# Optimization experiments

Hardware: AMD Instinct MI355X
Metric: run time of the kernel (lower is better)

The kernel has to match this reference:

```python
import jax, jax.numpy as jnp
import numpy as np

N = 8192
D_IN, D_H, D_OUT = 512, 256, 128
BETA = 0.8
EPS = 1e-08


def _xavier(key, fan_in, fan_out):
    limit = float(np.sqrt(6.0 / (fan_in + fan_out)))
    return jax.random.uniform(key, (fan_in, fan_out), jnp.float32, -limit, limit)


def setup_inputs() -> dict:
    key = jax.random.key(0)
    kA, kS, kx, kw1, kw2 = jax.random.split(key, 5)
    A = jax.random.uniform(kA, (N, N), jnp.float32)
    S = jax.random.uniform(kS, (N, N), jnp.float32)
    x = jax.random.normal(kx, (N, D_IN), jnp.float32)
    W1 = _xavier(kw1, D_IN, D_H)
    b1 = jnp.zeros((D_H,), jnp.float32)
    W2 = _xavier(kw2, D_H, D_OUT)
    b2 = jnp.zeros((D_OUT,), jnp.float32)
    return {"A": A, "S": S, "x": x, "W1": W1, "b1": b1, "W2": W2, "b2": b2}


def _normalize_adj(adj):
    # adj + eps * I  (add only on the diagonal; no dense eye materialized)
    idx = jnp.arange(adj.shape[0])
    adj = adj.at[idx, idx].add(EPS)
    d = adj.sum(axis=1)                       # [N]
    d_inv_sqrt = d ** -0.5
    d_inv_sqrt = jnp.where(jnp.isinf(d_inv_sqrt), 0.0, d_inv_sqrt)
    # D^{-1/2} A D^{-1/2} as broadcast row/col scaling (same math as diag matmuls)
    return d_inv_sqrt[:, None] * adj * d_inv_sqrt[None, :]


def reference(A, S, x, W1, b1, W2, b2):
    A_tilde = A + BETA * S                    # [N, N]
    A_norm = _normalize_adj(A_tilde)          # [N, N]
    # GCN layer 1: relu(A_norm @ (x @ W1) + b1)   (dropout is identity at eval)
    h = jax.nn.relu(A_norm @ (x @ W1) + b1)   # [N, D_H]
    # GCN layer 2 (output layer, no activation)
    out = A_norm @ (h @ W2) + b2              # [N, D_OUT]
    return out
```

## Files before the change

### kernel.cpp

```cpp
#include <hip/hip_runtime.h>

#define EPS 1e-8f
#define BETA 0.8f

typedef __attribute__((ext_vector_type(8))) short bf16x8;
typedef __attribute__((ext_vector_type(4))) float f32x4;
typedef __attribute__((ext_vector_type(4))) float float4v;
typedef __attribute__((ext_vector_type(4))) unsigned short ushort4v;

__device__ __forceinline__ unsigned short f2b(float f) {
  unsigned int u = __builtin_bit_cast(unsigned int, f);
  u += 0x7fffu + ((u >> 16) & 1u);
  return (unsigned short)(u >> 16);
}
__device__ __forceinline__ float b2f(unsigned short u) {
  unsigned int x = (unsigned int)u << 16;
  return __builtin_bit_cast(float, x);
}

__global__ __launch_bounds__(256) void k_degree_conv(
    const float* __restrict__ A, const float* __restrict__ S,
    unsigned short* __restrict__ At, float* __restrict__ dis,
    const float* __restrict__ x, unsigned short* __restrict__ xb,
    const float* __restrict__ W1, unsigned short* __restrict__ W1T,
    const float* __restrict__ W2, unsigned short* __restrict__ W2T) {
  __shared__ float wsum[4];
  const int tid = threadIdx.x;
  if (blockIdx.x < 8192) {
    const int row = blockIdx.x;
    const size_t base = (size_t)row * 8192;
    float4v a[8], s[8];
#pragma unroll
    for (int i = 0; i < 8; ++i) {
      const int c = i * 1024 + tid * 4;
      a[i] = __builtin_nontemporal_load(
          reinterpret_cast<const float4v*>(A + base + c));
      s[i] = __builtin_nontemporal_load(
          reinterpret_cast<const float4v*>(S + base + c));
    }
    float sum = 0.f;
#pragma unroll
    for (int i = 0; i < 8; ++i) {
      const int c = i * 1024 + tid * 4;
      float v0 = a[i].x + BETA * s[i].x;
      float v1 = a[i].y + BETA * s[i].y;
      float v2 = a[i].z + BETA * s[i].z;
      float v3 = a[i].w + BETA * s[i].w;
      sum += (v0 + v1) + (v2 + v3);
      ushort4v o = {f2b(v0), f2b(v1), f2b(v2), f2b(v3)};
      *reinterpret_cast<ushort4v*>(At + base + c) = o;
    }
#pragma unroll
    for (int off = 32; off > 0; off >>= 1) sum += __shfl_xor(sum, off, 64);
    if ((tid & 63) == 0) wsum[tid >> 6] = sum;
    __syncthreads();
    if (tid == 0) {
      float d = ((wsum[0] + wsum[1]) + (wsum[2] + wsum[3])) + EPS;
      dis[row] = (d > 0.f) ? 1.0f / sqrtf(d) : 0.f;
    }
  } else {
    const int b = blockIdx.x - 8192;
    if (b < 4096) {
      const int idx = b * 256 + tid;
      float4v v = reinterpret_cast<const float4v*>(x)[idx];
      ushort4v o = {f2b(v.x), f2b(v.y), f2b(v.z), f2b(v.w)};
      reinterpret_cast<ushort4v*>(xb)[idx] = o;
    } else if (b < 4608) {
      const int idx = (b - 4096) * 256 + tid;
      const int r = idx >> 8, c = idx & 255;
      W1T[c * 512 + r] = f2b(W1[idx]);
    } else {
      const int idx = (b - 4608) * 256 + tid;
      const int r = idx >> 7, c = idx & 127;
      W2T[c * 256 + r] = f2b(W2[idx]);
    }
  }
}

__global__ __launch_bounds__(256) void k_conv_all(
    const float* __restrict__ x, unsigned short* __restrict__ xb,
    const float* __restrict__ W1, unsigned short* __restrict__ W1T,
    const float* __restrict__ W2, unsigned short* __restrict__ W2T) {
  const int b = blockIdx.x;
  if (b < 4096) {
    const int idx = b * 256 + threadIdx.x;
    float4v v = reinterpret_cast<const float4v*>(x)[idx];
    ushort4v o = {f2b(v.x), f2b(v.y), f2b(v.z), f2b(v.w)};
    reinterpret_cast<ushort4v*>(xb)[idx] = o;
  } else if (b < 4608) {
    const int idx = (b - 4096) * 256 + threadIdx.x;
    const int r = idx >> 8, c = idx & 255;
    W1T[c * 512 + r] = f2b(W1[idx]);
  } else {
    const int idx = (b - 4608) * 256 + threadIdx.x;
    const int r = idx >> 7, c = idx & 127;
    W2T[c * 256 + r] = f2b(W2[idx]);
  }
}

__global__ __launch_bounds__(256) void k_degree_convert(
    const float* __restrict__ A, const float* __restrict__ S,
    unsigned short* __restrict__ At, float* __restrict__ dis) {
  const int row = blockIdx.x;
  const int tid = threadIdx.x;
  const size_t base = (size_t)row * 8192;
  float4v a[8], s[8];
#pragma unroll
  for (int i = 0; i < 8; ++i) {
    const int c = i * 1024 + tid * 4;
    a[i] = __builtin_nontemporal_load(
        reinterpret_cast<const float4v*>(A + base + c));
    s[i] = __builtin_nontemporal_load(
        reinterpret_cast<const float4v*>(S + base + c));
  }
  float sum = 0.f;
#pragma unroll
  for (int i = 0; i < 8; ++i) {
    const int c = i * 1024 + tid * 4;
    float v0 = a[i].x + BETA * s[i].x;
    float v1 = a[i].y + BETA * s[i].y;
    float v2 = a[i].z + BETA * s[i].z;
    float v3 = a[i].w + BETA * s[i].w;
    sum += (v0 + v1) + (v2 + v3);
    ushort4v o = {f2b(v0), f2b(v1), f2b(v2), f2b(v3)};
    *reinterpret_cast<ushort4v*>(At + base + c) = o;
  }
#pragma unroll
  for (int off = 32; off > 0; off >>= 1) sum += __shfl_xor(sum, off, 64);
  __shared__ float wsum[4];
  if ((tid & 63) == 0) wsum[tid >> 6] = sum;
  __syncthreads();
  if (tid == 0) {
    float d = ((wsum[0] + wsum[1]) + (wsum[2] + wsum[3])) + EPS;
    dis[row] = (d > 0.f) ? 1.0f / sqrtf(d) : 0.f;
  }
}

template <int BM, int BN, int EPI>
__global__ __launch_bounds__(256) void k_gemm_bt(
    const unsigned short* __restrict__ Ag, const unsigned short* __restrict__ BTg,
    int M, int N, int Kstride, int Kchunk,
    const float* __restrict__ dis, const float* __restrict__ bias,
    float* __restrict__ outf, unsigned short* __restrict__ outb) {
  constexpr int WM = BM / 2, WN = BN / 2;
  constexpr int MF = WM / 16, NF = WN / 16;
  constexpr int NLOADS = BM / 32 + BN / 32;
  __shared__ unsigned short Als[2][BM][64];
  __shared__ unsigned short Bls[2][BN][64];
  const int tid = threadIdx.x;
  const int lane = tid & 63;
  const int wm = (tid >> 6) >> 1, wn = (tid >> 6) & 1;
  const int brow = blockIdx.x * BM, bcol = blockIdx.y * BN;
  const int ar = tid >> 3;
  const int ac = (tid & 7) * 8;
  const int l15 = lane & 15, lk = (lane >> 4) * 8;

  f32x4 acc[MF][NF];
#pragma unroll
  for (int i = 0; i < MF; ++i)
#pragma unroll
    for (int j = 0; j < NF; ++j) acc[i][j] = (f32x4){0.f, 0.f, 0.f, 0.f};

  auto stage = [&](int buf, int k0) {
#pragma unroll
    for (int i = 0; i < BM / 32; ++i) {
      const unsigned short* g =
          Ag + (size_t)(brow + i * 32 + ar) * Kstride + k0 + ac;
      __builtin_amdgcn_global_load_lds(
          (const __attribute__((address_space(1))) void*)g,
          (__attribute__((address_space(3))) void*)&Als[buf][i * 32 + ar][ac],
          16, 0, 0);
    }
#pragma unroll
    for (int i = 0; i < BN / 32; ++i) {
      const unsigned short* g =
          BTg + (size_t)(bcol + i * 32 + ar) * Kstride + k0 + ac;
      __builtin_amdgcn_global_load_lds(
          (const __attribute__((address_space(1))) void*)g,
          (__attribute__((address_space(3))) void*)&Bls[buf][i * 32 + ar][ac],
          16, 0, 0);
    }
  };

  const int nsteps = Kchunk / 64;
  stage(0, 0);
  for (int t = 0; t < nsteps; ++t) {
    const int cur = t & 1;
    if (t + 1 < nsteps) {
      stage(cur ^ 1, (t + 1) * 64);
      asm volatile("s_waitcnt vmcnt(%0)" ::"n"(NLOADS));
    } else {
      asm volatile("s_waitcnt vmcnt(0)");
    }
    __builtin_amdgcn_s_barrier();
    asm volatile("" ::: "memory");
#pragma unroll
    for (int kk = 0; kk < 2; ++kk) {
      bf16x8 afr[MF], bfr[NF];
#pragma unroll
      for (int mi = 0; mi < MF; ++mi)
        afr[mi] = *reinterpret_cast<const bf16x8*>(
            &Als[cur][wm * WM + mi * 16 + l15][kk * 32 + lk]);
#pragma unroll
      for (int ni = 0; ni < NF; ++ni)
        bfr[ni] = *reinterpret_cast<const bf16x8*>(
            &Bls[cur][wn * WN + ni * 16 + l15][kk * 32 + lk]);
#pragma unroll
      for (int mi = 0; mi < MF; ++mi)
#pragma unroll
        for (int ni = 0; ni < NF; ++ni)
          acc[mi][ni] = __builtin_amdgcn_mfma_f32_16x16x32_bf16(
              afr[mi], bfr[ni], acc[mi][ni], 0, 0, 0);
    }
    asm volatile("" ::: "memory");
    __builtin_amdgcn_s_barrier();
  }

  const int crow0 = brow + wm * WM, ccol0 = bcol + wn * WN;
#pragma unroll
  for (int mi = 0; mi < MF; ++mi) {
    const int row0 = crow0 + mi * 16 + (lane >> 4) * 4;
    const float d0 = dis[row0], d1 = dis[row0 + 1], d2 = dis[row0 + 2],
                d3 = dis[row0 + 3];
#pragma unroll
    for (int ni = 0; ni < NF; ++ni) {
      const int col = ccol0 + ni * 16 + l15;
      f32x4 a = acc[mi][ni];
      if constexpr (EPI == 0) {
        ushort4v o = {f2b(d0 * a.x), f2b(d1 * a.y), f2b(d2 * a.z),
                      f2b(d3 * a.w)};
        *reinterpret_cast<ushort4v*>(outb + (size_t)col * M + row0) = o;
      } else if constexpr (EPI == 1) {
        const float bb = bias[col];
        float v0 = d0 * a.x + bb; v0 = v0 > 0.f ? v0 : 0.f;
        float v1 = d1 * a.y + bb; v1 = v1 > 0.f ? v1 : 0.f;
        float v2 = d2 * a.z + bb; v2 = v2 > 0.f ? v2 : 0.f;
        float v3 = d3 * a.w + bb; v3 = v3 > 0.f ? v3 : 0.f;
        outb[(size_t)(row0 + 0) * N + col] = f2b(v0);
        outb[(size_t)(row0 + 1) * N + col] = f2b(v1);
        outb[(size_t)(row0 + 2) * N + col] = f2b(v2);
        outb[(size_t)(row0 + 3) * N + col] = f2b(v3);
      } else {
        const float bb = bias[col];
        outf[(size_t)(row0 + 0) * N + col] = d0 * a.x + bb;
        outf[(size_t)(row0 + 1) * N + col] = d1 * a.y + bb;
        outf[(size_t)(row0 + 2) * N + col] = d2 * a.z + bb;
        outf[(size_t)(row0 + 3) * N + col] = d3 * a.w + bb;
      }
    }
  }
}

__global__ __launch_bounds__(512, 4) void k_gemm_big(
    const unsigned short* __restrict__ Ag,
    const unsigned short* __restrict__ BTg,
    int N, int Kchunk, int gx, int ncol,
    unsigned short* __restrict__ P) {
  constexpr int M = 8192, Kstride = 8192;
  constexpr int NLOADS = 4;
  __shared__ unsigned short Als[2][128][64];
  __shared__ unsigned short Bls[2][128][64];

  const int nblk = gridDim.x;
  const int flat = blockIdx.x;
  const int cpx = nblk >> 3;
  const int swz = (flat & 7) * cpx + (flat >> 3);
  const int bx = swz % gx;
  const int rem = swz / gx;
  const int by = rem % ncol;
  const int bz = rem / ncol;

  const int tid = threadIdx.x;
  const int lane = tid & 63;
  const int wid = tid >> 6;
  const int wm = wid >> 2, wn = wid & 3;
  const int brow = bx * 128;
  const int bcol = by * 128;
  const int kbase = bz * Kchunk;
  const int ar = tid >> 3;
  const int acs = ((tid & 7) ^ (ar & 7)) * 8;
  const int l15 = lane & 15;
  const int lk = (lane >> 4) * 8;
  const int rk = (l15 & 7) * 8;

  f32x4 acc[4][2];
#pragma unroll
  for (int i = 0; i < 4; ++i)
#pragma unroll
    for (int j = 0; j < 2; ++j) acc[i][j] = (f32x4){0.f, 0.f, 0.f, 0.f};

  auto stage = [&](int buf, int k0) {
#pragma unroll
    for (int i = 0; i < 2; ++i) {
      const unsigned short* g =
          Ag + (size_t)(brow + i * 64 + ar) * Kstride + k0 + acs;
      __builtin_amdgcn_global_load_lds(
          (const __attribute__((address_space(1))) void*)g,
          (__attribute__((address_space(3))) void*)
              &Als[buf][i * 64 + ar][(tid & 7) * 8],
          16, 0, 0);
    }
#pragma unroll
    for (int i = 0; i < 2; ++i) {
      const unsigned short* g =
          BTg + (size_t)(bcol + i * 64 + ar) * Kstride + k0 + acs;
      __builtin_amdgcn_global_load_lds(
          (const __attribute__((address_space(1))) void*)g,
          (__attribute__((address_space(3))) void*)
              &Bls[buf][i * 64 + ar][(tid & 7) * 8],
          16, 0, 0);
    }
  };

  const int nsteps = Kchunk / 64;
  stage(0, kbase);
  for (int t = 0; t < nsteps; ++t) {
    const int cur = t & 1;
    if (t + 1 < nsteps) {
      stage(cur ^ 1, kbase + (t + 1) * 64);
      asm volatile("s_waitcnt vmcnt(%0)" ::"n"(NLOADS));
    } else {
      asm volatile("s_waitcnt vmcnt(0)");
    }
    __builtin_amdgcn_s_barrier();
    asm volatile("" ::: "memory");
#pragma unroll
    for (int kk = 0; kk < 2; ++kk) {
      bf16x8 afr[4], bfr[2];
#pragma unroll
      for (int mi = 0; mi < 4; ++mi)
        afr[mi] = *reinterpret_cast<const bf16x8*>(
            &Als[cur][wm * 64 + mi * 16 + l15][(kk * 32 + lk) ^ rk]);
#pragma unroll
      for (int ni = 0; ni < 2; ++ni)
        bfr[ni] = *reinterpret_cast<const bf16x8*>(
            &Bls[cur][wn * 32 + ni * 16 + l15][(kk * 32 + lk) ^ rk]);
      __builtin_amdgcn_s_setprio(1);
#pragma unroll
      for (int mi = 0; mi < 4; ++mi)
#pragma unroll
        for (int ni = 0; ni < 2; ++ni)
          acc[mi][ni] = __builtin_amdgcn_mfma_f32_16x16x32_bf16(
              afr[mi], bfr[ni], acc[mi][ni], 0, 0, 0);
      __builtin_amdgcn_s_setprio(0);
    }
    asm volatile("" ::: "memory");
    __builtin_amdgcn_s_barrier();
  }

  unsigned short* Pz = P + (size_t)bz * M * N;
  const int crow0 = brow + wm * 64, ccol0 = bcol + wn * 32;
#pragma unroll
  for (int mi = 0; mi < 4; ++mi) {
    const int row0 = crow0 + mi * 16 + (lane >> 4) * 4;
#pragma unroll
    for (int ni = 0; ni < 2; ++ni) {
      const int col = ccol0 + ni * 16 + l15;
      f32x4 a = acc[mi][ni];
      Pz[(size_t)(row0 + 0) * N + col] = f2b(a.x);
      Pz[(size_t)(row0 + 1) * N + col] = f2b(a.y);
      Pz[(size_t)(row0 + 2) * N + col] = f2b(a.z);
      Pz[(size_t)(row0 + 3) * N + col] = f2b(a.w);
    }
  }
}

__global__ __launch_bounds__(256, 2) void k_h_gemm(
    const unsigned short* __restrict__ P,
    const unsigned short* __restrict__ W2T,
    const float* __restrict__ dis, const float* __restrict__ b1,
    unsigned short* __restrict__ M2T) {
  __shared__ unsigned short W2ls[128][256];
  __shared__ unsigned short hls[32][256];
  const int tid = threadIdx.x;
  const int lane = tid & 63;
  const int l15 = lane & 15;
  const int wid = tid >> 6;
  const int m0 = blockIdx.x * 32;

  {
    const int wr = tid >> 5, wc = tid & 31;
#pragma unroll
    for (int i = 0; i < 16; ++i) {
      const int row = i * 8 + wr;
      const unsigned short* g = W2T + row * 256 + ((wc ^ (row & 7)) * 8);
      __builtin_amdgcn_global_load_lds(
          (const __attribute__((address_space(1))) void*)g,
          (__attribute__((address_space(3))) void*)&W2ls[row][wc * 8], 16, 0,
          0);
    }
  }

  {
    const int col4 = (tid & 63) * 4;
    const int rsub = tid >> 6;
    const float4v bv = *reinterpret_cast<const float4v*>(b1 + col4);
    const int ch = (tid & 63) >> 1;
    const int sub = (tid & 1) * 4;
#pragma unroll
    for (int p = 0; p < 8; ++p) {
      const int row = p * 4 + rsub;
      const size_t off = (size_t)(m0 + row) * 256 + col4;
      float r0 = 0.f, r1 = 0.f, r2 = 0.f, r3 = 0.f;
#pragma unroll
      for (int z = 0; z < 4; ++z) {
        ushort4v v =
            *reinterpret_cast<const ushort4v*>(P + (size_t)z * 2097152 + off);
        r0 += b2f(v.x); r1 += b2f(v.y); r2 += b2f(v.z); r3 += b2f(v.w);
      }
      const float dm = dis[m0 + row];
      r0 = dm * r0 + bv.x;
      r1 = dm * r1 + bv.y;
      r2 = dm * r2 + bv.z;
      r3 = dm * r3 + bv.w;
      r0 = r0 > 0.f ? r0 : 0.f;
      r1 = r1 > 0.f ? r1 : 0.f;
      r2 = r2 > 0.f ? r2 : 0.f;
      r3 = r3 > 0.f ? r3 : 0.f;
      ushort4v o = {f2b(r0), f2b(r1), f2b(r2), f2b(r3)};
      *reinterpret_cast<ushort4v*>(
          &hls[row][(ch ^ (row & 7)) * 8 + sub]) = o;
    }
  }
  __syncthreads();

  f32x4 acc[2][2];
#pragma unroll
  for (int i = 0; i < 2; ++i)
#pragma unroll
    for (int j = 0; j < 2; ++j) acc[i][j] = (f32x4){0.f, 0.f, 0.f, 0.f};

#pragma unroll
  for (int kk = 0; kk < 8; ++kk) {
    const int gch = kk * 4 + (lane >> 4);
    bf16x8 a[2], b[2];
#pragma unroll
    for (int mi = 0; mi < 2; ++mi) {
      const int mr = mi * 16 + l15;
      a[mi] =
          *reinterpret_cast<const bf16x8*>(&hls[mr][(gch ^ (mr & 7)) * 8]);
    }
#pragma unroll
    for (int ni = 0; ni < 2; ++ni) {
      const int nr = wid * 32 + ni * 16 + l15;
      b[ni] =
          *reinterpret_cast<const bf16x8*>(&W2ls[nr][(gch ^ (nr & 7)) * 8]);
    }
#pragma unroll
    for (int mi = 0; mi < 2; ++mi)
#pragma unroll
      for (int ni = 0; ni < 2; ++ni)
        acc[mi][ni] = __builtin_amdgcn_mfma_f32_16x16x32_bf16(
            a[mi], b[ni], acc[mi][ni], 0, 0, 0);
  }

#pragma unroll
  for (int mi = 0; mi < 2; ++mi) {
    const int r0 = mi * 16 + (lane >> 4) * 4;
    const float d0 = dis[m0 + r0], d1 = dis[m0 + r0 + 1],
                d2 = dis[m0 + r0 + 2], d3 = dis[m0 + r0 + 3];
#pragma unroll
    for (int ni = 0; ni < 2; ++ni) {
      const int col = wid * 32 + ni * 16 + l15;
      f32x4 a = acc[mi][ni];
      ushort4v o = {f2b(d0 * a.x), f2b(d1 * a.y), f2b(d2 * a.z),
                    f2b(d3 * a.w)};
      *reinterpret_cast<ushort4v*>(&M2T[(size_t)col * 8192 + m0 + r0]) = o;
    }
  }
}

template <int NS>
__global__ __launch_bounds__(256) void k_reduceN(
    const unsigned short* __restrict__ P, int M, int N,
    const float* __restrict__ dis, const float* __restrict__ bias,
    float* __restrict__ outf) {
  const int idx = blockIdx.x * 256 + threadIdx.x;
  const int row = idx / (N / 4);
  const int c0 = (idx - row * (N / 4)) * 4;
  const size_t off = (size_t)row * N + c0;
  const size_t ps = (size_t)M * N;
  float r0 = 0.f, r1 = 0.f, r2 = 0.f, r3 = 0.f;
#pragma unroll
  for (int z = 0; z < NS; ++z) {
    ushort4v v = *reinterpret_cast<const ushort4v*>(P + z * ps + off);
    r0 += b2f(v.x); r1 += b2f(v.y); r2 += b2f(v.z); r3 += b2f(v.w);
  }
  const float d = dis[row];
  float4v bb = *reinterpret_cast<const float4v*>(bias + c0);
  float4v o = {d * r0 + bb.x, d * r1 + bb.y, d * r2 + bb.z, d * r3 + bb.w};
  *reinterpret_cast<float4v*>(outf + off) = o;
}

extern "C" void kernel_launch(void* const* d_in, const int* in_sizes, int n_in,
                              void* d_out, int out_size, void* d_ws,
                              size_t ws_size, hipStream_t stream) {
  const float* A  = (const float*)d_in[0];
  const float* S  = (const float*)d_in[1];
  const float* x  = (const float*)d_in[2];
  const float* W1 = (const float*)d_in[3];
  const float* b1 = (const float*)d_in[4];
  const float* W2 = (const float*)d_in[5];
  const float* b2 = (const float*)d_in[6];
  float* out = (float*)d_out;

  char* ws = (char*)d_ws;
  dim3 blk(256);

  const size_t O_At = 0, O_xb = 134217728, O_M1T = 142606336,
               O_P = 146800640, O_W1T = 180355072, O_W2T = 180617216,
               O_dis = 180682752, NEED = 180715520;

  if (ws_size >= NEED) {
    unsigned short* At  = (unsigned short*)(ws + O_At);
    unsigned short* xb  = (unsigned short*)(ws + O_xb);
    unsigned short* M1T = (unsigned short*)(ws + O_M1T);
    unsigned short* P   = (unsigned short*)(ws + O_P);
    unsigned short* M2T = (unsigned short*)(ws + O_xb);
    unsigned short* W1T = (unsigned short*)(ws + O_W1T);
    unsigned short* W2T = (unsigned short*)(ws + O_W2T);
    float*          dis = (float*)(ws + O_dis);

    k_degree_conv<<<12928, blk, 0, stream>>>(A, S, At, dis, x, xb, W1, W1T,
                                             W2, W2T);
    k_gemm_bt<128, 64, 0><<<dim3(64, 4), blk, 0, stream>>>(
        xb, W1T, 8192, 256, 512, 512, dis, nullptr, nullptr, M1T);
    k_gemm_big<<<dim3(512), dim3(512), 0, stream>>>(At, M1T, 256, 2048, 64, 2,
                                                    P);
    k_h_gemm<<<256, blk, 0, stream>>>(P, W2T, dis, b1, M2T);
    k_gemm_big<<<dim3(512), dim3(512), 0, stream>>>(At, M2T, 128, 1024, 64, 1,
                                                    P);
    k_reduceN<8><<<1024, blk, 0, stream>>>(P, 8192, 128, dis, b2, out);
  } else {
    unsigned short* At  = (unsigned short*)(ws);
    unsigned short* xb  = (unsigned short*)(ws + 134217728);
    unsigned short* M1T = (unsigned short*)(ws + 142606336);
    unsigned short* hb  = (unsigned short*)(ws + 146800640);
    unsigned short* M2T = (unsigned short*)(ws + 150994944);
    unsigned short* W1T = (unsigned short*)(ws + 153092096);
    unsigned short* W2T = (unsigned short*)(ws + 153354240);
    float* dis          = (float*)(ws + 153419776);

    k_degree_convert<<<8192, blk, 0, stream>>>(A, S, At, dis);
    k_conv_all<<<4736, blk, 0, stream>>>(x, xb, W1, W1T, W2, W2T);
    k_gemm_bt<128, 64, 0><<<dim3(64, 4), blk, 0, stream>>>(
        xb, W1T, 8192, 256, 512, 512, dis, nullptr, nullptr, M1T);
    k_gemm_bt<128, 64, 1><<<dim3(64, 4), blk, 0, stream>>>(
        At, M1T, 8192, 256, 8192, 8192, dis, b1, nullptr, hb);
    k_gemm_bt<64, 64, 0><<<dim3(128, 2), blk, 0, stream>>>(
        hb, W2T, 8192, 128, 256, 256, dis, nullptr, nullptr, M2T);
    k_gemm_bt<64, 64, 2><<<dim3(128, 2), blk, 0, stream>>>(
        At, M2T, 8192, 128, 8192, 8192, dis, b2, out, nullptr);
  }
}
```

Measured before the change: 196.3 us.

## Fuse split-K reductions into big GEMMs via last-block atomic counters

Folds the layer-1 split-K reduction, bias, ReLU and h@W2 GEMM into the tail of the first big GEMM, and the layer-2 split-K reduction plus bias into the second. A per-row-tile atomic counter picks the last-arriving block to do the reduction, which removes two kernel launches and a separate pass over the partial buffers. The cost is a memset, atomics with fences, and serial tail work done by only 64 blocks. The fused h@W2 step reads W2T straight from global memory rather than staging it in LDS.

```diff
diff --git a/kernel.cpp b/kernel.cpp
--- a/kernel.cpp
+++ b/kernel.cpp
@@ -251,24 +251,26 @@
   }
 }
 
-__global__ __launch_bounds__(512, 4) void k_gemm_big(
+__global__ __launch_bounds__(512, 4) void k_gemm_l1(
     const unsigned short* __restrict__ Ag,
     const unsigned short* __restrict__ BTg,
-    int N, int Kchunk, int gx, int ncol,
-    unsigned short* __restrict__ P) {
-  constexpr int M = 8192, Kstride = 8192;
+    unsigned short* __restrict__ P,
+    const unsigned short* __restrict__ W2T,
+    const float* __restrict__ dis, const float* __restrict__ b1,
+    unsigned short* __restrict__ M2T,
+    int* __restrict__ cnt) {
+  constexpr int Kstride = 8192, N = 256, Kchunk = 2048, gx = 64;
   constexpr int NLOADS = 4;
-  __shared__ unsigned short Als[2][128][64];
-  __shared__ unsigned short Bls[2][128][64];
-
-  const int nblk = gridDim.x;
+  __shared__ unsigned short smem[2][2][128][64];
+  __shared__ int lastf;
+
   const int flat = blockIdx.x;
-  const int cpx = nblk >> 3;
+  const int cpx = 64;
   const int swz = (flat & 7) * cpx + (flat >> 3);
   const int bx = swz % gx;
   const int rem = swz / gx;
-  const int by = rem % ncol;
-  const int bz = rem / ncol;
+  const int by = rem & 1;
+  const int bz = rem >> 1;
 
   const int tid = threadIdx.x;
   const int lane = tid & 63;
@@ -297,7 +299,7 @@
       __builtin_amdgcn_global_load_lds(
           (const __attribute__((address_space(1))) void*)g,
           (__attribute__((address_space(3))) void*)
-              &Als[buf][i * 64 + ar][(tid & 7) * 8],
+              &smem[0][buf][i * 64 + ar][(tid & 7) * 8],
           16, 0, 0);
     }
 #pragma unroll
@@ -307,7 +309,7 @@
       __builtin_amdgcn_global_load_lds(
           (const __attribute__((address_space(1))) void*)g,
           (__attribute__((address_space(3))) void*)
-              &Bls[buf][i * 64 + ar][(tid & 7) * 8],
+              &smem[1][buf][i * 64 + ar][(tid & 7) * 8],
           16, 0, 0);
     }
   };
@@ -330,11 +332,11 @@
 #pragma unroll
       for (int mi = 0; mi < 4; ++mi)
         afr[mi] = *reinterpret_cast<const bf16x8*>(
-            &Als[cur][wm * 64 + mi * 16 + l15][(kk * 32 + lk) ^ rk]);
+            &smem[0][cur][wm * 64 + mi * 16 + l15][(kk * 32 + lk) ^ rk]);
 #pragma unroll
       for (int ni = 0; ni < 2; ++ni)
         bfr[ni] = *reinterpret_cast<const bf16x8*>(
-            &Bls[cur][wn * 32 + ni * 16 + l15][(kk * 32 + lk) ^ rk]);
+            &smem[1][cur][wn * 32 + ni * 16 + l15][(kk * 32 + lk) ^ rk]);
       __builtin_amdgcn_s_setprio(1);
 #pragma unroll
       for (int mi = 0; mi < 4; ++mi)
@@ -348,7 +350,7 @@
     __builtin_amdgcn_s_barrier();
   }
 
-  unsigned short* Pz = P + (size_t)bz * M * N;
+  unsigned short* Pz = P + (size_t)bz * 2097152;
   const int crow0 = brow + wm * 64, ccol0 = bcol + wn * 32;
 #pragma unroll
   for (int mi = 0; mi < 4; ++mi) {
@@ -363,133 +365,231 @@
       Pz[(size_t)(row0 + 3) * N + col] = f2b(a.w);
     }
   }
-}
-
-__global__ __launch_bounds__(256, 2) void k_h_gemm(
-    const unsigned short* __restrict__ P,
-    const unsigned short* __restrict__ W2T,
-    const float* __restrict__ dis, const float* __restrict__ b1,
-    unsigned short* __restrict__ M2T) {
-  __shared__ unsigned short W2ls[128][256];
-  __shared__ unsigned short hls[32][256];
+
+  __syncthreads();
+  if (tid == 0) {
+    __threadfence();
+    int r = atomicAdd(&cnt[bx], 1);
+    __threadfence();
+    lastf = (r == 7) ? 1 : 0;
+  }
+  __syncthreads();
+  if (!lastf) return;
+
+  unsigned short(*hls)[256] =
+      reinterpret_cast<unsigned short(*)[256]>(&smem[0][0][0][0]);
+#pragma unroll
+  for (int i = 0; i < 16; ++i) {
+    const int fi = tid + i * 512;
+    const int row = fi >> 6;
+    const int c4 = (fi & 63) * 4;
+    const size_t off = (size_t)(brow + row) * 256 + c4;
+    float r0 = 0.f, r1 = 0.f, r2 = 0.f, r3 = 0.f;
+#pragma unroll
+    for (int z = 0; z < 4; ++z) {
+      ushort4v v =
+          *reinterpret_cast<const ushort4v*>(P + (size_t)z * 2097152 + off);
+      r0 += b2f(v.x); r1 += b2f(v.y); r2 += b2f(v.z); r3 += b2f(v.w);
+    }
+    const float dm = dis[brow + row];
+    const float4v bv = *reinterpret_cast<const float4v*>(b1 + c4);
+    r0 = dm * r0 + bv.x; r1 = dm * r1 + bv.y;
+    r2 = dm * r2 + bv.z; r3 = dm * r3 + bv.w;
+    r0 = r0 > 0.f ? r0 : 0.f;
+    r1 = r1 > 0.f ? r1 : 0.f;
+    r2 = r2 > 0.f ? r2 : 0.f;
+    r3 = r3 > 0.f ? r3 : 0.f;
+    const int ch = c4 >> 3, sub = c4 & 7;
+    ushort4v o = {f2b(r0), f2b(r1), f2b(r2), f2b(r3)};
+    *reinterpret_cast<ushort4v*>(&hls[row][((ch ^ (row & 7)) << 3) + sub]) = o;
+  }
+  __syncthreads();
+
+  const int m0w = (wid >> 1) * 32;
+  const int n0w = (wid & 1) * 64;
+  f32x4 acc2[2][4];
+#pragma unroll
+  for (int i = 0; i < 2; ++i)
+#pragma unroll
+    for (int j = 0; j < 4; ++j) acc2[i][j] = (f32x4){0.f, 0.f, 0.f, 0.f};
+#pragma unroll
+  for (int kk = 0; kk < 8; ++kk) {
+    const int gch = kk * 4 + (lane >> 4);
+    bf16x8 a2[2], b2v[4];
+#pragma unroll
+    for (int mi = 0; mi < 2; ++mi) {
+      const int mr = m0w + mi * 16 + l15;
+      a2[mi] = *reinterpret_cast<const bf16x8*>(
+          &hls[mr][((gch ^ (mr & 7)) << 3)]);
+    }
+#pragma unroll
+    for (int ni = 0; ni < 4; ++ni) {
+      const int nr = n0w + ni * 16 + l15;
+      b2v[ni] = *reinterpret_cast<const bf16x8*>(W2T + nr * 256 + gch * 8);
+    }
+#pragma unroll
+    for (int mi = 0; mi < 2; ++mi)
+#pragma unroll
+      for (int ni = 0; ni < 4; ++ni)
+        acc2[mi][ni] = __builtin_amdgcn_mfma_f32_16x16x32_bf16(
+            a2[mi], b2v[ni], acc2[mi][ni], 0, 0, 0);
+  }
+#pragma unroll
+  for (int mi = 0; mi < 2; ++mi) {
+    const int r0 = m0w + mi * 16 + (lane >> 4) * 4;
+    const float d0 = dis[brow + r0], d1 = dis[brow + r0 + 1],
+                d2 = dis[brow + r0 + 2], d3 = dis[brow + r0 + 3];
+#pragma unroll
+    for (int ni = 0; ni < 4; ++ni) {
+      const int col = n0w + ni * 16 + l15;
+      f32x4 a = acc2[mi][ni];
+      ushort4v o = {f2b(d0 * a.x), f2b(d1 * a.y), f2b(d2 * a.z),
+                    f2b(d3 * a.w)};
+      *reinterpret_cast<ushort4v*>(&M2T[(size_t)col * 8192 + brow + r0]) = o;
+    }
+  }
+}
+
+__global__ __launch_bounds__(512, 4) void k_gemm_l2(
+    const unsigned short* __restrict__ Ag,
+    const unsigned short* __restrict__ BTg,
+    unsigned short* __restrict__ P,
+    const float* __restrict__ dis, const float* __restrict__ b2,
+    float* __restrict__ out,
+    int* __restrict__ cnt) {
+  constexpr int Kstride = 8192, N = 128, Kchunk = 1024, gx = 64;
+  constexpr int NLOADS = 4;
+  __shared__ unsigned short Als[2][128][64];
+  __shared__ unsigned short Bls[2][128][64];
+  __shared__ int lastf;
+
+  const int flat = blockIdx.x;
+  const int swz = (flat & 7) * 64 + (flat >> 3);
+  const int bx = swz % gx;
+  const int bz = swz / gx;
+
   const int tid = threadIdx.x;
   const int lane = tid & 63;
+  const int wid = tid >> 6;
+  const int wm = wid >> 2, wn = wid & 3;
+  const int brow = bx * 128;
+  const int kbase = bz * Kchunk;
+  const int ar = tid >> 3;
+  const int acs = ((tid & 7) ^ (ar & 7)) * 8;
   const int l15 = lane & 15;
-  const int wid = tid >> 6;
-  const int m0 = blockIdx.x * 32;
-
-  {
-    const int wr = tid >> 5, wc = tid & 31;
-#pragma unroll
-    for (int i = 0; i < 16; ++i) {
-      const int row = i * 8 + wr;
-      const unsigned short* g = W2T + row * 256 + ((wc ^ (row & 7)) * 8);
+  const int lk = (lane >> 4) * 8;
+  const int rk = (l15 & 7) * 8;
+
+  f32x4 acc[4][2];
+#pragma unroll
+  for (int i = 0; i < 4; ++i)
+#pragma unroll
+    for (int j = 0; j < 2; ++j) acc[i][j] = (f32x4){0.f, 0.f, 0.f, 0.f};
+
+  auto stage = [&](int buf, int k0) {
+#pragma unroll
+    for (int i = 0; i < 2; ++i) {
+      const unsigned short* g =
+          Ag + (size_t)(brow + i * 64 + ar) * Kstride + k0 + acs;
       __builtin_amdgcn_global_load_lds(
           (const __attribute__((address_space(1))) void*)g,
-          (__attribute__((address_space(3))) void*)&W2ls[row][wc * 8], 16, 0,
-          0);
-    }
-  }
-
-  {
-    const int col4 = (tid & 63) * 4;
-    const int rsub = tid >> 6;
-    const float4v bv = *reinterpret_cast<const float4v*>(b1 + col4);
-    const int ch = (tid & 63) >> 1;
-    const int sub = (tid & 1) * 4;
-#pragma unroll
-    for (int p = 0; p < 8; ++p) {
-      const int row = p * 4 + rsub;
-      const size_t off = (size_t)(m0 + row) * 256 + col4;
-      float r0 = 0.f, r1 = 0.f, r2 = 0.f, r3 = 0.f;
-#pragma unroll
-      for (int z = 0; z < 4; ++z) {
-        ushort4v v =
-            *reinterpret_cast<const ushort4v*>(P + (size_t)z * 2097152 + off);
-        r0 += b2f(v.x); r1 += b2f(v.y); r2 += b2f(v.z); r3 += b2f(v.w);
-      }
-      const float dm = dis[m0 + row];
-      r0 = dm * r0 + bv.x;
-      r1 = dm * r1 + bv.y;
-      r2 = dm * r2 + bv.z;
-      r3 = dm * r3 + bv.w;
-      r0 = r0 > 0.f ? r0 : 0.f;
-      r1 = r1 > 0.f ? r1 : 0.f;
-      r2 = r2 > 0.f ? r2 : 0.f;
-      r3 = r3 > 0.f ? r3 : 0.f;
-      ushort4v o = {f2b(r0), f2b(r1), f2b(r2), f2b(r3)};
-      *reinterpret_cast<ushort4v*>(
-          &hls[row][(ch ^ (row & 7)) * 8 + sub]) = o;
-    }
-  }
+          (__attribute__((address_space(3))) void*)
+              &Als[buf][i * 64 + ar][(tid & 7) * 8],
+          16, 0, 0);
+    }
+#pragma unroll
+    for (int i = 0; i < 2; ++i) {
+      const unsigned short* g =
+          BTg + (size_t)(i * 64 + ar) * Kstride + k0 + acs;
+      __builtin_amdgcn_global_load_lds(
+          (const __attribute__((address_space(1))) void*)g,
+          (__attribute__((address_space(3))) void*)
+              &Bls[buf][i * 64 + ar][(tid & 7) * 8],
+          16, 0, 0);
+    }
+  };
+
+  const int nsteps = Kchunk / 64;
+  stage(0, kbase);
+  for (int t = 0; t < nsteps; ++t) {
+    const int cur = t & 1;
+    if (t + 1 < nsteps) {
+      stage(cur ^ 1, kbase + (t + 1) * 64);
+      asm volatile("s_waitcnt vmcnt(%0)" ::"n"(NLOADS));
+    } else {
+      asm volatile("s_waitcnt vmcnt(0)");
+    }
+    __builtin_amdgcn_s_barrier();
+    asm volatile("" ::: "memory");
+#pragma unroll
+    for (int kk = 0; kk < 2; ++kk) {
+      bf16x8 afr[4], bfr[2];
+#pragma unroll
+      for (int mi = 0; mi < 4; ++mi)
+        afr[mi] = *reinterpret_cast<const bf16x8*>(
+            &Als[cur][wm * 64 + mi * 16 + l15][(kk * 32 + lk) ^ rk]);
+#pragma unroll
+      for (int ni = 0; ni < 2; ++ni)
+        bfr[ni] = *reinterpret_cast<const bf16x8*>(
+            &Bls[cur][wn * 32 + ni * 16 + l15][(kk * 32 + lk) ^ rk]);
+      __builtin_amdgcn_s_setprio(1);
+#pragma unroll
+      for (int mi = 0; mi < 4; ++mi)
+#pragma unroll
+        for (int ni = 0; ni < 2; ++ni)
+          acc[mi][ni] = __builtin_amdgcn_mfma_f32_16x16x32_bf16(
+              afr[mi], bfr[ni], acc[mi][ni], 0, 0, 0);
+      __builtin_amdgcn_s_setprio(0);
+    }
+    asm volatile("" ::: "memory");
+    __builtin_amdgcn_s_barrier();
+  }
+
+  unsigned short* Pz = P + (size_t)bz * 1048576;
+  const int crow0 = brow + wm * 64, ccol0 = wn * 32;
+#pragma unroll
+  for (int mi = 0; mi < 4; ++mi) {
+    const int row0 = crow0 + mi * 16 + (lane >> 4) * 4;
+#pragma unroll
+    for (int ni = 0; ni < 2; ++ni) {
+      const int col = ccol0 + ni * 16 + l15;
+      f32x4 a = acc[mi][ni];
+      Pz[(size_t)(row0 + 0) * N + col] = f2b(a.x);
+      Pz[(size_t)(row0 + 1) * N + col] = f2b(a.y);
+      Pz[(size_t)(row0 + 2) * N + col] = f2b(a.z);
+      Pz[(size_t)(row0 + 3) * N + col] = f2b(a.w);
+    }
+  }
+
   __syncthreads();
-
-  f32x4 acc[2][2];
-#pragma unroll
-  for (int i = 0; i < 2; ++i)
-#pragma unroll
-    for (int j = 0; j < 2; ++j) acc[i][j] = (f32x4){0.f, 0.f, 0.f, 0.f};
-
-#pragma unroll
-  for (int kk = 0; kk < 8; ++kk) {
-    const int gch = kk * 4 + (lane >> 4);
-    bf16x8 a[2], b[2];
-#pragma unroll
-    for (int mi = 0; mi < 2; ++mi) {
-      const int mr = mi * 16 + l15;
-      a[mi] =
-          *reinterpret_cast<const bf16x8*>(&hls[mr][(gch ^ (mr & 7)) * 8]);
-    }
-#pragma unroll
-    for (int ni = 0; ni < 2; ++ni) {
-      const int nr = wid * 32 + ni * 16 + l15;
-      b[ni] =
-          *reinterpret_cast<const bf16x8*>(&W2ls[nr][(gch ^ (nr & 7)) * 8]);
-    }
-#pragma unroll
-    for (int mi = 0; mi < 2; ++mi)
-#pragma unroll
-      for (int ni = 0; ni < 2; ++ni)
-        acc[mi][ni] = __builtin_amdgcn_mfma_f32_16x16x32_bf16(
-            a[mi], b[ni], acc[mi][ni], 0, 0, 0);
-  }
-
-#pragma unroll
-  for (int mi = 0; mi < 2; ++mi) {
-    const int r0 = mi * 16 + (lane >> 4) * 4;
-    const float d0 = dis[m0 + r0], d1 = dis[m0 + r0 + 1],
-                d2 = dis[m0 + r0 + 2], d3 = dis[m0 + r0 + 3];
-#pragma unroll
-    for (int ni = 0; ni < 2; ++ni) {
-      const int col = wid * 32 + ni * 16 + l15;
-      f32x4 a = acc[mi][ni];
-      ushort4v o = {f2b(d0 * a.x), f2b(d1 * a.y), f2b(d2 * a.z),
-                    f2b(d3 * a.w)};
-      *reinterpret_cast<ushort4v*>(&M2T[(size_t)col * 8192 + m0 + r0]) = o;
-    }
-  }
-}
-
-template <int NS>
-__global__ __launch_bounds__(256) void k_reduceN(
-    const unsigned short* __restrict__ P, int M, int N,
-    const float* __restrict__ dis, const float* __restrict__ bias,
-    float* __restrict__ outf) {
-  const int idx = blockIdx.x * 256 + threadIdx.x;
-  const int row = idx / (N / 4);
-  const int c0 = (idx - row * (N / 4)) * 4;
-  const size_t off = (size_t)row * N + c0;
-  const size_t ps = (size_t)M * N;
-  float r0 = 0.f, r1 = 0.f, r2 = 0.f, r3 = 0.f;
-#pragma unroll
-  for (int z = 0; z < NS; ++z) {
-    ushort4v v = *reinterpret_cast<const ushort4v*>(P + z * ps + off);
-    r0 += b2f(v.x); r1 += b2f(v.y); r2 += b2f(v.z); r3 += b2f(v.w);
-  }
-  const float d = dis[row];
-  float4v bb = *reinterpret_cast<const float4v*>(bias + c0);
-  float4v o = {d * r0 + bb.x, d * r1 + bb.y, d * r2 + bb.z, d * r3 + bb.w};
-  *reinterpret_cast<float4v*>(outf + off) = o;
+  if (tid == 0) {
+    __threadfence();
+    int r = atomicAdd(&cnt[bx], 1);
+    __threadfence();
+    lastf = (r == 7) ? 1 : 0;
+  }
+  __syncthreads();
+  if (!lastf) return;
+
+#pragma unroll
+  for (int i = 0; i < 8; ++i) {
+    const int fi = tid + i * 512;
+    const int row = fi >> 5;
+    const int c4 = (fi & 31) * 4;
+    const size_t off = (size_t)(brow + row) * 128 + c4;
+    float r0 = 0.f, r1 = 0.f, r2 = 0.f, r3 = 0.f;
+#pragma unroll
+    for (int z = 0; z < 8; ++z) {
+      ushort4v v =
+          *reinterpret_cast<const ushort4v*>(P + (size_t)z * 1048576 + off);
+      r0 += b2f(v.x); r1 += b2f(v.y); r2 += b2f(v.z); r3 += b2f(v.w);
+    }
+    const float dm = dis[brow + row];
+    const float4v bv = *reinterpret_cast<const float4v*>(b2 + c4);
+    float4v o = {dm * r0 + bv.x, dm * r1 + bv.y, dm * r2 + bv.z,
+                 dm * r3 + bv.w};
+    *reinterpret_cast<float4v*>(out + off) = o;
+  }
 }
 
 extern "C" void kernel_launch(void* const* d_in, const int* in_sizes, int n_in,
@@ -509,7 +609,7 @@
 
   const size_t O_At = 0, O_xb = 134217728, O_M1T = 142606336,
                O_P = 146800640, O_W1T = 180355072, O_W2T = 180617216,
-               O_dis = 180682752, NEED = 180715520;
+               O_dis = 180682752, O_cnt = 180715520, NEED = 180716544;
 
   if (ws_size >= NEED) {
     unsigned short* At  = (unsigned short*)(ws + O_At);
@@ -520,17 +620,17 @@
     unsigned short* W1T = (unsigned short*)(ws + O_W1T);
     unsigned short* W2T = (unsigned short*)(ws + O_W2T);
     float*          dis = (float*)(ws + O_dis);
-
+    int*            cnt = (int*)(ws + O_cnt);
+
+    hipMemsetAsync(cnt, 0, 512, stream);
     k_degree_conv<<<12928, blk, 0, stream>>>(A, S, At, dis, x, xb, W1, W1T,
                                              W2, W2T);
     k_gemm_bt<128, 64, 0><<<dim3(64, 4), blk, 0, stream>>>(
         xb, W1T, 8192, 256, 512, 512, dis, nullptr, nullptr, M1T);
-    k_gemm_big<<<dim3(512), dim3(512), 0, stream>>>(At, M1T, 256, 2048, 64, 2,
-                                                    P);
-    k_h_gemm<<<256, blk, 0, stream>>>(P, W2T, dis, b1, M2T);
-    k_gemm_big<<<dim3(512), dim3(512), 0, stream>>>(At, M2T, 128, 1024, 64, 1,
-                                                    P);
-    k_reduceN<8><<<1024, blk, 0, stream>>>(P, 8192, 128, dis, b2, out);
+    k_gemm_l1<<<dim3(512), dim3(512), 0, stream>>>(At, M1T, P, W2T, dis, b1,
+                                                   M2T, cnt);
+    k_gemm_l2<<<dim3(512), dim3(512), 0, stream>>>(At, M2T, P, dis, b2, out,
+                                                   cnt + 64);
   } else {
     unsigned short* At  = (unsigned short*)(ws);
     unsigned short* xb  = (unsigned short*)(ws + 134217728);
```

New measurement: 295.6 us. 50.6% more time.
